# Optimization experiments

Hardware: AMD Instinct MI355X
Metric: run time of the kernel (lower is better)

The kernel has to match this reference:

```python
import jax, jax.numpy as jnp
import numpy as np


def setup_inputs() -> dict:
    key = jax.random.key(0)
    k1, k2, k3, k4, k5 = jax.random.split(key, 5)
    out_f, in_f, group_size = 11008, 4096, 128
    n_groups = in_f // group_size  # 32
    x = jax.random.normal(k1, (32, in_f), dtype=jnp.float16)
    packed = jax.random.randint(k2, (out_f, in_f // 2), 0, 256, dtype=jnp.int32)
    scales = (jax.random.uniform(k3, (out_f, n_groups), dtype=jnp.float32) * 0.02 + 0.001).astype(jnp.float16)
    zeros = (jax.random.normal(k4, (out_f, n_groups), dtype=jnp.float32) * 0.05).astype(jnp.float16)
    bias = (jax.random.normal(k5, (out_f,), dtype=jnp.float32) * 0.02).astype(jnp.float16)
    return {"x": x, "packed": packed, "scales": scales, "zeros": zeros,
            "bias": bias, "group_size": group_size, "in_features": in_f}


def _dequantize(packed, scales, zeros, in_features, group_size):
    # packed: [out_f, padded_in//2] uint8-valued ints; two int4 nibbles per byte.
    out_f = packed.shape[0]
    padded_in = packed.shape[1] * 2
    high = (packed >> 4) & 15
    low = packed & 15
    # interleave: even columns = high nibble, odd columns = low nibble
    unpacked = jnp.stack([high, low], axis=-1).reshape(out_f, padded_in).astype(scales.dtype)
    n_groups = scales.shape[1]
    grouped = unpacked.reshape(out_f, n_groups, group_size)
    deq = grouped * scales[:, :, None] + zeros[:, :, None]
    return deq.reshape(out_f, padded_in)[:, :in_features].astype(jnp.float16)


def reference(x, packed, scales, zeros, bias, group_size, in_features):
    # Fused dequant + linear: y = x @ W^T + b, with W reconstructed from int4.
    weight = _dequantize(packed, scales, zeros, in_features, group_size)  # [out_f, in_f]
    out = jnp.dot(x, weight.T) + bias
    return out
```

## Files before the change

kernel.cpp:

```cpp
#include <hip/hip_runtime.h>
#include <hip/hip_fp16.h>
#include <hip/hip_bf16.h>

typedef unsigned int u32;
typedef unsigned short u16;
typedef short short8 __attribute__((ext_vector_type(8)));
typedef float f32x4 __attribute__((ext_vector_type(4)));

#define IN_F 4096
#define OUT_F 11008
#define MROWS 32
#define CCOLS 2048
#define NGRP 32
#define KSPL 8
#define NBX (OUT_F / 64)
#define XFRAG_BYTES ((size_t)MROWS * IN_F * 2)
#define SZ_BYTES ((size_t)NGRP * OUT_F * 4)
#define SF_OFF XFRAG_BYTES
#define ZA_OFF (SF_OFF + SZ_BYTES)
#define PART_OFF (ZA_OFF + SZ_BYTES)
#define PART_BYTES ((size_t)KSPL * MROWS * OUT_F * 4)
#define WS_NEED (PART_OFF + PART_BYTES)

typedef const __attribute__((address_space(1))) void* gas_t;
typedef __attribute__((address_space(3))) void* las_t;
__device__ __forceinline__ void gl_lds16(const void* g, void* l) {
  __builtin_amdgcn_global_load_lds((gas_t)g, (las_t)l, 16, 0, 0);
}

__device__ __forceinline__ float bf2f(u16 b) {
  u32 t = ((u32)b) << 16;
  return __builtin_bit_cast(float, t);
}
__device__ __forceinline__ u32 f2bf_rne(float f) {
  u32 b = __builtin_bit_cast(u32, f);
  return (b + 0x7FFFu + ((b >> 16) & 1u)) >> 16;
}
__device__ __forceinline__ float h2f(u16 h) {
  return __half2float(__builtin_bit_cast(__half, h));
}

__device__ __forceinline__ u32 detect_mode(const u16* sc) {
  int l = (int)(threadIdx.x & 63u);
  u16 u = sc[2 * l];
  int e = (u >> 7) & 0xFF;
  unsigned long long mA = __ballot(e >= 114 && e <= 124);
  unsigned long long mC = __ballot(e >= 36 && e <= 88);
  int cA = __popcll(mA), cC = __popcll(mC);
  return (cA >= 48) ? 0u : ((cC >= 48) ? 2u : 1u);
}

__device__ __forceinline__ float ld_sz(const void* p, int idx, u32 mode) {
  if (mode == 0) return bf2f(((const u16*)p)[idx]);
  if (mode == 2) return h2f(((const u16*)p)[idx]);
  return ((const float*)p)[idx];
}

__device__ __forceinline__ u32 deq2(u32 v, float sf, float za) {
  float uh = __builtin_bit_cast(float, 0x43000000u | ((v << 12) & 0xF0000u));
  float ul = __builtin_bit_cast(float, 0x43000000u | ((v << 16) & 0xF0000u));
  float wh = __builtin_fmaf(uh, sf, za);
  float wl = __builtin_fmaf(ul, sf, za);
  __hip_bfloat162 pk = __float22bfloat162_rn(make_float2(wh, wl));
  u32 r;
  __builtin_memcpy(&r, &pk, 4);
  return r;
}
__device__ __forceinline__ uint4 deq4(uint4 bv, float sf, float za) {
  uint4 r;
  r.x = deq2(bv.x, sf, za); r.y = deq2(bv.y, sf, za);
  r.z = deq2(bv.z, sf, za); r.w = deq2(bv.w, sf, za);
  return r;
}

__device__ __forceinline__ uint4 lda8(const void* x, int eoff, u32 mode) {
  if (mode == 0) return *reinterpret_cast<const uint4*>((const u16*)x + eoff);
  if (mode == 1) {
    float4 u = *reinterpret_cast<const float4*>((const float*)x + eoff);
    float4 v = *reinterpret_cast<const float4*>((const float*)x + eoff + 4);
    uint4 r;
    r.x = f2bf_rne(u.x) | (f2bf_rne(u.y) << 16);
    r.y = f2bf_rne(u.z) | (f2bf_rne(u.w) << 16);
    r.z = f2bf_rne(v.x) | (f2bf_rne(v.y) << 16);
    r.w = f2bf_rne(v.z) | (f2bf_rne(v.w) << 16);
    return r;
  }
  uint4 h = *reinterpret_cast<const uint4*>((const u16*)x + eoff);
  uint4 r;
  r.x = f2bf_rne(h2f((u16)(h.x & 0xFFFF))) | (f2bf_rne(h2f((u16)(h.x >> 16))) << 16);
  r.y = f2bf_rne(h2f((u16)(h.y & 0xFFFF))) | (f2bf_rne(h2f((u16)(h.y >> 16))) << 16);
  r.z = f2bf_rne(h2f((u16)(h.z & 0xFFFF))) | (f2bf_rne(h2f((u16)(h.z >> 16))) << 16);
  r.w = f2bf_rne(h2f((u16)(h.w & 0xFFFF))) | (f2bf_rne(h2f((u16)(h.w >> 16))) << 16);
  return r;
}

__global__ __launch_bounds__(256) void qz_prep(
    const void* __restrict__ x, const void* __restrict__ scales,
    const void* __restrict__ zeros, u16* __restrict__ xfrag,
    float* __restrict__ sfT, float* __restrict__ zaT) {
  const u32 mode = detect_mode((const u16*)scales);
  const int t = (int)blockIdx.x * 256 + (int)threadIdx.x;
  if (t < 16384) {
    const int s = t >> 7, h = (t >> 6) & 1, lane = t & 63;
    const int q = lane & 15, p = lane >> 4;
    const int src = (h * 16 + q) * IN_F + s * 32 + p * 8;
    *reinterpret_cast<uint4*>(xfrag + (size_t)t * 8) = lda8(x, src, mode);
  } else {
    const int u = t - 16384;
    if (u < NGRP * OUT_F) {
      const int g = u / OUT_F, o = u - g * OUT_F;
      const float sfv = ld_sz(scales, o * NGRP + g, mode);
      const float zfv = ld_sz(zeros, o * NGRP + g, mode);
      sfT[u] = sfv;
      zaT[u] = zfv - 128.0f * sfv;
    }
  }
}

__global__ __launch_bounds__(256, 4) void qv_gemm(
    const u16* __restrict__ xfrag, const int* __restrict__ packed,
    const float* __restrict__ sfT, const float* __restrict__ zaT,
    float* __restrict__ part) {
  __shared__ __align__(16) char smem[4][8][1024];
  const int tid = (int)threadIdx.x;
  const int lane = tid & 63, wid = tid >> 6;
  const int q = lane & 15, p = lane >> 4;
  const int o0 = (int)blockIdx.x * 64 + wid * 16;
  const int ksl = (int)blockIdx.y;
  const int o = o0 + q;
  const int k32_0 = ksl * 16;

  const int g0 = ksl * 4;
  float sf[4], za[4];
#pragma unroll
  for (int g = 0; g < 4; ++g) {
    sf[g] = sfT[(size_t)(g0 + g) * OUT_F + o];
    za[g] = zaT[(size_t)(g0 + g) * OUT_F + o];
  }
  asm volatile("" ::: "memory");

  const uint4* xf = reinterpret_cast<const uint4*>(xfrag);
  uint4 a0[8], a1[8];
#pragma unroll
  for (int s = 0; s < 8; ++s) {
    a0[s] = xf[(size_t)((k32_0 + s) * 2 + 0) * 64 + lane];
    a1[s] = xf[(size_t)((k32_0 + s) * 2 + 1) * 64 + lane];
  }
  asm volatile("" ::: "memory");

  const int br = lane >> 2, bc = lane & 3;
  const int* bsrc = packed + (size_t)(o0 + br) * CCOLS + k32_0 * 16
                    + ((bc ^ ((br >> 1) & 3)) << 2);
#pragma unroll
  for (int s = 0; s < 8; ++s) {
    gl_lds16(bsrc + s * 16, &smem[wid][s][0]);
    asm volatile("" ::: "memory");
  }

  f32x4 acc0 = {0.f, 0.f, 0.f, 0.f}, acc1 = {0.f, 0.f, 0.f, 0.f};
  const int rdoff = q * 64 + ((p ^ ((q >> 1) & 3)) << 4);

#define QCOMP(S, W, SFI)                                                      \
  {                                                                           \
    asm volatile("s_waitcnt vmcnt(" #W ")" ::: "memory");                     \
    const uint4 bv = *reinterpret_cast<const uint4*>(&smem[wid][S][rdoff]);   \
    const uint4 bw = deq4(bv, sf[SFI], za[SFI]);                              \
    acc0 = __builtin_amdgcn_mfma_f32_16x16x32_bf16(                           \
        __builtin_bit_cast(short8, a0[S]), __builtin_bit_cast(short8, bw),    \
        acc0, 0, 0, 0);                                                       \
    acc1 = __builtin_amdgcn_mfma_f32_16x16x32_bf16(                           \
        __builtin_bit_cast(short8, a1[S]), __builtin_bit_cast(short8, bw),    \
        acc1, 0, 0, 0);                                                       \
  }
#define QFILL(S)                                                              \
  {                                                                           \
    gl_lds16(bsrc + (8 + S) * 16, &smem[wid][S][0]);                          \
    a0[S] = xf[(size_t)((k32_0 + 8 + S) * 2 + 0) * 64 + lane];                \
    a1[S] = xf[(size_t)((k32_0 + 8 + S) * 2 + 1) * 64 + lane];                \
  }

  QCOMP(0, 7, 0)  QFILL(0)
  QCOMP(1, 9, 0)  QFILL(1)
  QCOMP(2, 11, 0) QFILL(2)
  QCOMP(3, 13, 0) QFILL(3)
  QCOMP(4, 15, 1) QFILL(4)
  QCOMP(5, 17, 1) QFILL(5)
  QCOMP(6, 19, 1) QFILL(6)
  QCOMP(7, 21, 1) QFILL(7)

  QCOMP(0, 21, 2)
  QCOMP(1, 18, 2)
  QCOMP(2, 15, 2)
  QCOMP(3, 12, 2)
  QCOMP(4, 9, 3)
  QCOMP(5, 6, 3)
  QCOMP(6, 3, 3)
  QCOMP(7, 0, 3)
#undef QCOMP
#undef QFILL

  float* base = part + ((size_t)(ksl * NBX + (int)blockIdx.x) * 4 + wid) * 512
                + lane * 8;
  *reinterpret_cast<f32x4*>(base) = acc0;
  *reinterpret_cast<f32x4*>(base + 4) = acc1;
}

__global__ __launch_bounds__(256) void qr_reduce(
    const float* __restrict__ part, const void* __restrict__ scales,
    const void* __restrict__ bias, void* __restrict__ out) {
  const u32 mode = detect_mode((const u16*)scales);
  const int bx = (int)blockIdx.x;
  const int wid = (int)threadIdx.x >> 6, lane = (int)threadIdx.x & 63;
  const int q = lane & 15, p = lane >> 4;
  const int o = bx * 64 + wid * 16 + q;

  float s0[4] = {0.f, 0.f, 0.f, 0.f}, s1[4] = {0.f, 0.f, 0.f, 0.f};
#pragma unroll
  for (int ksl = 0; ksl < KSPL; ++ksl) {
    const float* base = part + ((size_t)(ksl * NBX + bx) * 4 + wid) * 512 + lane * 8;
    const float4 v0 = *reinterpret_cast<const float4*>(base);
    const float4 v1 = *reinterpret_cast<const float4*>(base + 4);
    s0[0] += v0.x; s0[1] += v0.y; s0[2] += v0.z; s0[3] += v0.w;
    s1[0] += v1.x; s1[1] += v1.y; s1[2] += v1.z; s1[3] += v1.w;
  }
  const float bb = ld_sz(bias, o, mode);
#pragma unroll
  for (int rr = 0; rr < 4; ++rr) {
    const float v0 = s0[rr] + bb, v1 = s1[rr] + bb;
    const size_t i0 = (size_t)(p * 4 + rr) * OUT_F + o;
    const size_t i1 = (size_t)(16 + p * 4 + rr) * OUT_F + o;
    if (mode == 1) {
      ((float*)out)[i0] = v0; ((float*)out)[i1] = v1;
    } else {
      ((u16*)out)[i0] = (u16)f2bf_rne(v0);
      ((u16*)out)[i1] = (u16)f2bf_rne(v1);
    }
  }
}

__global__ __launch_bounds__(256, 4) void qp_direct(
    const void* __restrict__ xsrc, const int* __restrict__ packed,
    const void* __restrict__ scales, const void* __restrict__ zeros,
    const void* __restrict__ bias, void* __restrict__ out) {
  constexpr int NSTEP = 128;
  constexpr int BD = 8, AD = 4;
  const u32 mode = detect_mode((const u16*)scales);
  const int tid = (int)threadIdx.x;
  const int lane = tid & 63, wid = tid >> 6;
  const int q = lane & 15, p = lane >> 4;
  const int tile = (int)blockIdx.x * 4 + wid;
  const int o = tile * 16 + q;
  const int* pr = packed + (size_t)o * CCOLS + p * 4;
  const int ae0 = q * IN_F + p * 8;
  const int ae1 = ae0 + 16 * IN_F;
  uint4 bb[BD], a0[AD], a1[AD];
#pragma unroll
  for (int i = 0; i < BD; ++i) bb[i] = *reinterpret_cast<const uint4*>(pr + i * 16);
#pragma unroll
  for (int i = 0; i < AD; ++i) {
    a0[i] = lda8(xsrc, ae0 + i * 32, mode);
    a1[i] = lda8(xsrc, ae1 + i * 32, mode);
  }
  f32x4 acc0 = {0.f, 0.f, 0.f, 0.f}, acc1 = {0.f, 0.f, 0.f, 0.f};
  for (int g = 0; g < NSTEP / 4; ++g) {
    const float sf = ld_sz(scales, o * NGRP + g, mode);
    const float za = ld_sz(zeros, o * NGRP + g, mode) - 128.0f * sf;
#pragma unroll
    for (int u = 0; u < 4; ++u) {
      const int s = g * 4 + u;
      const uint4 bw = deq4(bb[s % BD], sf, za);
      const uint4 av0 = a0[s % AD], av1 = a1[s % AD];
      if (s + BD < NSTEP) bb[s % BD] = *reinterpret_cast<const uint4*>(pr + (s + BD) * 16);
      if (s + AD < NSTEP) {
        a0[s % AD] = lda8(xsrc, ae0 + (s + AD) * 32, mode);
        a1[s % AD] = lda8(xsrc, ae1 + (s + AD) * 32, mode);
      }
      acc0 = __builtin_amdgcn_mfma_f32_16x16x32_bf16(
          __builtin_bit_cast(short8, av0), __builtin_bit_cast(short8, bw), acc0, 0, 0, 0);
      acc1 = __builtin_amdgcn_mfma_f32_16x16x32_bf16(
          __builtin_bit_cast(short8, av1), __builtin_bit_cast(short8, bw), acc1, 0, 0, 0);
    }
  }
  const float bbv = ld_sz(bias, o, mode);
#pragma unroll
  for (int r = 0; r < 4; ++r) {
    const float v0 = acc0[r] + bbv, v1 = acc1[r] + bbv;
    const size_t i0 = (size_t)(p * 4 + r) * OUT_F + o;
    const size_t i1 = (size_t)(16 + p * 4 + r) * OUT_F + o;
    if (mode == 1) { ((float*)out)[i0] = v0; ((float*)out)[i1] = v1; }
    else { ((u16*)out)[i0] = (u16)f2bf_rne(v0); ((u16*)out)[i1] = (u16)f2bf_rne(v1); }
  }
}

extern "C" void kernel_launch(void* const* d_in, const int* in_sizes, int n_in,
                              void* d_out, int out_size, void* d_ws, size_t ws_size,
                              hipStream_t stream) {
  (void)in_sizes; (void)n_in; (void)out_size;
  const void* x      = d_in[0];
  const int* packed  = (const int*)d_in[1];
  const void* scales = d_in[2];
  const void* zeros  = d_in[3];
  const void* bias   = d_in[4];

  if (ws_size >= WS_NEED) {
    u16* xfrag = (u16*)d_ws;
    float* sfT = (float*)((char*)d_ws + SF_OFF);
    float* zaT = (float*)((char*)d_ws + ZA_OFF);
    float* part = (float*)((char*)d_ws + PART_OFF);
    qz_prep<<<1440, 256, 0, stream>>>(x, scales, zeros, xfrag, sfT, zaT);
    qv_gemm<<<dim3(NBX, KSPL), 256, 0, stream>>>(xfrag, packed, sfT, zaT, part);
    qr_reduce<<<NBX, 256, 0, stream>>>(part, scales, bias, d_out);
  } else {
    qp_direct<<<OUT_F / 64, 256, 0, stream>>>(x, packed, scales, zeros, bias, d_out);
  }
}
```

Before: 37.73 us.

## Stage shared activation fragments in LDS and ring-buffer weight tiles

Activation fragments for the block's K slice are no longer loaded into registers separately by each of the four waves. They are now loaded once per block into LDS via direct global-to-LDS copies, with each wave loading a quarter, and a block barrier before compute. The weight tile buffer shrinks to a 4-deep ring per wave, and the fill/compute schedule is reworked around it. This cuts redundant global activation traffic and register pressure, but adds a barrier, extra LDS reads per MFMA step, and lowers the occupancy hint from 4 to 3 blocks per CU.

```diff
diff --git a/kernel.cpp b/kernel.cpp
--- a/kernel.cpp
+++ b/kernel.cpp
@@ -117,11 +117,12 @@
   }
 }
 
-__global__ __launch_bounds__(256, 4) void qv_gemm(
+__global__ __launch_bounds__(256, 3) void qv_gemm(
     const u16* __restrict__ xfrag, const int* __restrict__ packed,
     const float* __restrict__ sfT, const float* __restrict__ zaT,
     float* __restrict__ part) {
-  __shared__ __align__(16) char smem[4][8][1024];
+  __shared__ __align__(16) char smemA[32768];
+  __shared__ __align__(16) char smemB[4][4][1024];
   const int tid = (int)threadIdx.x;
   const int lane = tid & 63, wid = tid >> 6;
   const int q = lane & 15, p = lane >> 4;
@@ -139,12 +140,15 @@
   }
   asm volatile("" ::: "memory");
 
-  const uint4* xf = reinterpret_cast<const uint4*>(xfrag);
-  uint4 a0[8], a1[8];
-#pragma unroll
-  for (int s = 0; s < 8; ++s) {
-    a0[s] = xf[(size_t)((k32_0 + s) * 2 + 0) * 64 + lane];
-    a1[s] = xf[(size_t)((k32_0 + s) * 2 + 1) * 64 + lane];
+#pragma unroll
+  for (int j = 0; j < 4; ++j) {
+#pragma unroll
+    for (int h = 0; h < 2; ++h) {
+      const int s_loc = wid * 4 + j;
+      const int sg = k32_0 + s_loc;
+      gl_lds16(xfrag + ((size_t)(sg * 2 + h) * 64 + lane) * 8,
+               &smemA[(s_loc * 2 + h) * 1024]);
+    }
   }
   asm volatile("" ::: "memory");
 
@@ -152,52 +156,51 @@
   const int* bsrc = packed + (size_t)(o0 + br) * CCOLS + k32_0 * 16
                     + ((bc ^ ((br >> 1) & 3)) << 2);
 #pragma unroll
-  for (int s = 0; s < 8; ++s) {
-    gl_lds16(bsrc + s * 16, &smem[wid][s][0]);
+  for (int s = 0; s < 4; ++s) {
+    gl_lds16(bsrc + s * 16, &smemB[wid][s][0]);
     asm volatile("" ::: "memory");
   }
+
+  asm volatile("s_waitcnt vmcnt(4)" ::: "memory");
+  __builtin_amdgcn_s_barrier();
+  __builtin_amdgcn_sched_barrier(0);
 
   f32x4 acc0 = {0.f, 0.f, 0.f, 0.f}, acc1 = {0.f, 0.f, 0.f, 0.f};
   const int rdoff = q * 64 + ((p ^ ((q >> 1) & 3)) << 4);
 
-#define QCOMP(S, W, SFI)                                                      \
+#define QC(S, W, SFI)                                                         \
   {                                                                           \
     asm volatile("s_waitcnt vmcnt(" #W ")" ::: "memory");                     \
-    const uint4 bv = *reinterpret_cast<const uint4*>(&smem[wid][S][rdoff]);   \
+    const uint4 bv =                                                          \
+        *reinterpret_cast<const uint4*>(&smemB[wid][(S) & 3][rdoff]);         \
+    const uint4 av0 =                                                         \
+        *reinterpret_cast<const uint4*>(&smemA[(S)*2048 + lane * 16]);        \
+    const uint4 av1 =                                                         \
+        *reinterpret_cast<const uint4*>(&smemA[(S)*2048 + 1024 + lane * 16]); \
     const uint4 bw = deq4(bv, sf[SFI], za[SFI]);                              \
     acc0 = __builtin_amdgcn_mfma_f32_16x16x32_bf16(                           \
-        __builtin_bit_cast(short8, a0[S]), __builtin_bit_cast(short8, bw),    \
+        __builtin_bit_cast(short8, av0), __builtin_bit_cast(short8, bw),      \
         acc0, 0, 0, 0);                                                       \
     acc1 = __builtin_amdgcn_mfma_f32_16x16x32_bf16(                           \
-        __builtin_bit_cast(short8, a1[S]), __builtin_bit_cast(short8, bw),    \
+        __builtin_bit_cast(short8, av1), __builtin_bit_cast(short8, bw),      \
         acc1, 0, 0, 0);                                                       \
-  }
-#define QFILL(S)                                                              \
+    asm volatile("" ::: "memory");                                            \
+  }
+#define QF(T)                                                                 \
   {                                                                           \
-    gl_lds16(bsrc + (8 + S) * 16, &smem[wid][S][0]);                          \
-    a0[S] = xf[(size_t)((k32_0 + 8 + S) * 2 + 0) * 64 + lane];                \
-    a1[S] = xf[(size_t)((k32_0 + 8 + S) * 2 + 1) * 64 + lane];                \
-  }
-
-  QCOMP(0, 7, 0)  QFILL(0)
-  QCOMP(1, 9, 0)  QFILL(1)
-  QCOMP(2, 11, 0) QFILL(2)
-  QCOMP(3, 13, 0) QFILL(3)
-  QCOMP(4, 15, 1) QFILL(4)
-  QCOMP(5, 17, 1) QFILL(5)
-  QCOMP(6, 19, 1) QFILL(6)
-  QCOMP(7, 21, 1) QFILL(7)
-
-  QCOMP(0, 21, 2)
-  QCOMP(1, 18, 2)
-  QCOMP(2, 15, 2)
-  QCOMP(3, 12, 2)
-  QCOMP(4, 9, 3)
-  QCOMP(5, 6, 3)
-  QCOMP(6, 3, 3)
-  QCOMP(7, 0, 3)
-#undef QCOMP
-#undef QFILL
+    gl_lds16(bsrc + (T)*16, &smemB[wid][(T) & 3][0]);                         \
+    asm volatile("" ::: "memory");                                            \
+  }
+
+  QC(0, 3, 0)  QF(4)   QC(1, 3, 0)  QF(5)
+  QC(2, 3, 0)  QF(6)   QC(3, 3, 0)  QF(7)
+  QC(4, 3, 1)  QF(8)   QC(5, 3, 1)  QF(9)
+  QC(6, 3, 1)  QF(10)  QC(7, 3, 1)  QF(11)
+  QC(8, 3, 2)  QF(12)  QC(9, 3, 2)  QF(13)
+  QC(10, 3, 2) QF(14)  QC(11, 3, 2) QF(15)
+  QC(12, 3, 3) QC(13, 2, 3) QC(14, 1, 3) QC(15, 0, 3)
+#undef QC
+#undef QF
 
   float* base = part + ((size_t)(ksl * NBX + (int)blockIdx.x) * 4 + wid) * 512
                 + lane * 8;
```

Measured after the change: 34.08 us. 9.7% less time.
